# Optimization experiments

Measured on AMD Instinct MI355X. Metric: run time of the kernel, lower is better.

## Reference

```python
import jax, jax.numpy as jnp
import numpy as np

B, F, H, N, S, L, E = 32, 128, 256, 2048, 3, 2, 262144
DEG = E // (B * N)  # average degree used to normalize position updates


def setup_inputs() -> dict:
    key = jax.random.key(0)
    ks = jax.random.split(key, 12)
    s = 0.05
    return {
        "x": jax.random.normal(ks[0], (B, F), jnp.float32),
        "positions": jax.random.normal(ks[1], (N, S), jnp.float32),
        "W_in": jax.random.normal(ks[2], (F, H), jnp.float32) * s,
        "b_in": jnp.zeros((H,), jnp.float32),
        "Wg1": jax.random.normal(ks[3], (3, H // 2), jnp.float32) * s,
        "bg1": jnp.zeros((H // 2,), jnp.float32),
        "Wg2": jax.random.normal(ks[4], (H // 2, H), jnp.float32) * s,
        "bg2": jnp.zeros((H,), jnp.float32),
        "Wm": jax.random.normal(ks[5], (L, 2 * H + 1, H), jnp.float32) * s,
        "bm": jnp.zeros((L, H), jnp.float32),
        "Wu": jax.random.normal(ks[6], (L, 2 * H, H), jnp.float32) * s,
        "bu": jnp.zeros((L, H), jnp.float32),
        "Wp": jax.random.normal(ks[7], (L, H, 1), jnp.float32) * s,
        "W_out": jax.random.normal(ks[8], (H, 1), jnp.float32) * s,
        "b_out": jnp.zeros((1,), jnp.float32),
        "edge_index": jax.random.randint(ks[9], (2, E), 0, B * N, dtype=jnp.int32),
    }


def _geometric_features(positions, Wg1, bg1, Wg2, bg2):
    # For single points, pairwise / centroid / Hausdorff distances all reduce to
    # the euclidean distance, so feature[i, 0..2] = mean_{j != i} ||p_i - p_j||.
    n = positions.shape[0]
    diff = positions[:, None, :] - positions[None, :, :]      # [N, N, S]
    dsq = jnp.sum(diff * diff, axis=-1)                        # [N, N]
    mask = 1.0 - jnp.eye(n, dtype=positions.dtype)
    d = jnp.sqrt(jnp.where(mask > 0, dsq, 1.0)) * mask         # grad-safe sqrt
    mean_d = jnp.sum(d, axis=1) / (n - 1)                      # [N]
    gf = jnp.stack([mean_d, mean_d, mean_d], axis=-1)          # [N, 3]
    return jax.nn.relu(gf @ Wg1 + bg1) @ Wg2 + bg2             # [N, H]


def _forward(x, positions, W_in, b_in, Wg1, bg1, Wg2, bg2, Wm, bm, Wu, bu, Wp, W_out, b_out, edge_index):
    nn_ = B * N
    h = x @ W_in + b_in                                        # [B, H]
    h = jnp.broadcast_to(h[:, None, :], (B, N, H)).reshape(nn_, H)
    pos = jnp.broadcast_to(positions[None], (B, N, S)).reshape(nn_, S)
    g = _geometric_features(positions, Wg1, bg1, Wg2, bg2)     # [N, H]
    h = h + jnp.broadcast_to(g[None], (B, N, H)).reshape(nn_, H)
    src, dst = edge_index[0], edge_index[1]
    for l in range(L):  # small fixed layer loop
        dvec = pos[src] - pos[dst]
        d = jnp.sqrt(jnp.sum(dvec * dvec, axis=-1, keepdims=True) + 1e-12)  # [E, 1]
        m = jax.nn.relu(jnp.concatenate([h[src], h[dst], d], axis=-1) @ Wm[l] + bm[l])
        agg = jax.ops.segment_sum(m, dst, num_segments=nn_)    # [B*N, H]
        coef = m @ Wp[l]                                       # [E, 1]
        pos = pos + jax.ops.segment_sum((pos[dst] - pos[src]) * coef, dst, num_segments=nn_) / DEG
        h = h + jax.nn.relu(jnp.concatenate([h, agg], axis=-1) @ Wu[l] + bu[l])
    out = (h.reshape(B, N, H) @ W_out + b_out).squeeze(-1)     # [B, N]
    return out


def reference(x, positions, W_in, b_in, Wg1, bg1, Wg2, bg2, Wm, bm, Wu, bu, Wp, W_out, b_out, edge_index):
    return _forward(x, positions, W_in, b_in, Wg1, bg1, Wg2, bg2, Wm, bm, Wu, bu, Wp, W_out, b_out, edge_index)
```

## Files before the change

kernel.cpp:

```cpp
#include <hip/hip_runtime.h>
#include <math.h>

#define B_ 32
#define F_ 128
#define H_ 256
#define N_ 2048
#define L_ 2
#define E_ 262144
#define NN_ 65536

typedef __attribute__((ext_vector_type(8))) short short8;
typedef __attribute__((ext_vector_type(4))) float f32x4;
typedef __attribute__((ext_vector_type(2))) float f32x2;

static __device__ __forceinline__ unsigned short f2bf(float f) {
  unsigned int u = __float_as_uint(f);
  u += 0x7FFF + ((u >> 16) & 1);
  return (unsigned short)(u >> 16);
}
static __device__ __forceinline__ float bf2f(unsigned short u) {
  return __uint_as_float(((unsigned int)u) << 16);
}
static __device__ __forceinline__ unsigned int pk_bf16(float lo, float hi) {
  unsigned int r;
  asm("v_cvt_pk_bf16_f32 %0, %1, %2" : "=v"(r) : "v"(lo), "v"(hi));
  return r;
}

typedef const __attribute__((address_space(1))) unsigned int* as1p;
typedef __attribute__((address_space(3))) unsigned int* as3p;
static __device__ __forceinline__ void gload16(const void* g, void* l) {
  __builtin_amdgcn_global_load_lds((as1p)g, (as3p)l, 16, 0, 0);
}


__global__ void h0_kernel(const float* __restrict__ x, const float* __restrict__ W_in,
                          const float* __restrict__ b_in, float* __restrict__ h0) {
  int b = blockIdx.x;
  int j = threadIdx.x;
  float acc = b_in[j];
#pragma unroll 8
  for (int k = 0; k < F_; ++k)
    acc += x[b * F_ + k] * W_in[k * H_ + j];
  h0[b * H_ + j] = acc;
}

__global__ void meand_g_kernel(const float* __restrict__ positions,
                               const float* __restrict__ Wg1, const float* __restrict__ bg1,
                               const float* __restrict__ Wg2, const float* __restrict__ bg2,
                               float* __restrict__ g) {
  __shared__ float red[256];
  __shared__ float hid[128];
  int n = blockIdx.x;
  int t = threadIdx.x;
  float px = positions[n * 3 + 0], py = positions[n * 3 + 1], pz = positions[n * 3 + 2];
  float s = 0.f;
  for (int j = t; j < N_; j += 256) {
    float dx = px - positions[j * 3 + 0];
    float dy = py - positions[j * 3 + 1];
    float dz = pz - positions[j * 3 + 2];
    s += sqrtf(dx * dx + dy * dy + dz * dz);
  }
  red[t] = s;
  __syncthreads();
  for (int off = 128; off > 0; off >>= 1) {
    if (t < off) red[t] += red[t + off];
    __syncthreads();
  }
  float md = red[0] / (float)(N_ - 1);
  if (t < 128) {
    float w = Wg1[t] + Wg1[128 + t] + Wg1[256 + t];
    hid[t] = fmaxf(md * w + bg1[t], 0.f);
  }
  __syncthreads();
  float acc = bg2[t];
#pragma unroll 8
  for (int k = 0; k < 128; ++k)
    acc += hid[k] * Wg2[k * H_ + t];
  g[n * H_ + t] = acc;
}

__global__ void hbfinit_kernel(const float* __restrict__ h0, const float* __restrict__ g,
                               unsigned short* __restrict__ hbf) {
  int idx = blockIdx.x * blockDim.x + threadIdx.x;
  int row = idx >> 5;
  int c8 = (idx & 31) << 3;
  const float* hp = h0 + (row >> 11) * H_ + c8;
  const float* gp = g + (row & (N_ - 1)) * H_ + c8;
  const float4 a = *(const float4*)hp;
  const float4 a2 = *(const float4*)(hp + 4);
  const float4 b = *(const float4*)gp;
  const float4 b2 = *(const float4*)(gp + 4);
  short8 v;
  v[0] = (short)f2bf(a.x + b.x);  v[1] = (short)f2bf(a.y + b.y);
  v[2] = (short)f2bf(a.z + b.z);  v[3] = (short)f2bf(a.w + b.w);
  v[4] = (short)f2bf(a2.x + b2.x); v[5] = (short)f2bf(a2.y + b2.y);
  v[6] = (short)f2bf(a2.z + b2.z); v[7] = (short)f2bf(a2.w + b2.w);
  *(short8*)(hbf + (((size_t)row) << 8) + c8) = v;
}

__global__ void posinit_kernel(const float* __restrict__ positions, float* __restrict__ pos4) {
  int n = blockIdx.x * blockDim.x + threadIdx.x;
  int src = (n & (N_ - 1)) * 3;
  float4 v;
  v.x = positions[src + 0];
  v.y = positions[src + 1];
  v.z = positions[src + 2];
  v.w = 0.f;
  *(float4*)(pos4 + ((size_t)n << 2)) = v;
}


__global__ void deg_kernel(const int* __restrict__ ei, int* __restrict__ deg) {
  int e = blockIdx.x * 256 + threadIdx.x;
  atomicAdd(&deg[ei[E_ + e]], 1);
}

__global__ void scan1_kernel(const int* __restrict__ deg, int* __restrict__ bsum) {
  __shared__ int red[256];
  int t = threadIdx.x;
  red[t] = deg[blockIdx.x * 256 + t];
  __syncthreads();
  for (int off = 128; off > 0; off >>= 1) {
    if (t < off) red[t] += red[t + off];
    __syncthreads();
  }
  if (t == 0) bsum[blockIdx.x] = red[0];
}

__global__ void scan2_kernel(int* __restrict__ bsum) {
  __shared__ int s[256];
  int t = threadIdx.x;
  s[t] = bsum[t];
  __syncthreads();
  for (int off = 1; off < 256; off <<= 1) {
    int v = (t >= off) ? s[t - off] : 0;
    __syncthreads();
    s[t] += v;
    __syncthreads();
  }
  bsum[t] = (t == 0) ? 0 : s[t - 1];
}

__global__ void scan3_kernel(const int* __restrict__ deg, const int* __restrict__ bsum,
                             int* __restrict__ cur, int* __restrict__ rowptr) {
  __shared__ int s[256];
  int t = threadIdx.x;
  int i = blockIdx.x * 256 + t;
  s[t] = deg[i];
  __syncthreads();
  for (int off = 1; off < 256; off <<= 1) {
    int v = (t >= off) ? s[t - off] : 0;
    __syncthreads();
    s[t] += v;
    __syncthreads();
  }
  int excl = (t == 0) ? 0 : s[t - 1];
  int v = bsum[blockIdx.x] + excl;
  cur[i] = v;
  rowptr[i] = v;
}

__global__ void scatter_kernel(const int* __restrict__ ei, int* __restrict__ cur,
                               int* __restrict__ src_s) {
  int e = blockIdx.x * 256 + threadIdx.x;
  int s = ei[e], d = ei[E_ + e];
  int p = atomicAdd(&cur[d], 1);
  src_s[p] = s;
}

__global__ void wconv_all(const float* __restrict__ Wm, const float* __restrict__ Wu,
                          unsigned short* __restrict__ Wt1, unsigned short* __restrict__ Wut) {
  int idx = blockIdx.x * 256 + threadIdx.x;
  int sel = idx >> 14;
  int rem = idx & 16383;
  if (sel < 2) {
    const float* W = Wm + (size_t)sel * 513 * H_;
    unsigned short* dst = Wt1 + (size_t)sel * 131072 + ((size_t)rem << 3);
    int g = rem >> 13;
    int r2 = rem & 8191;
    int kc = r2 >> 11, w = (r2 >> 9) & 3, ks = (r2 >> 8) & 1, ni = (r2 >> 6) & 3, lane = r2 & 63;
    int r = lane & 15, q = lane >> 4;
    int n  = (w << 6) + (ni << 4) + r;
    int kb = (g << 8) + (kc << 6) + (ks << 5) + (q << 3);
#pragma unroll
    for (int j = 0; j < 8; ++j)
      dst[j] = f2bf(W[(size_t)(kb + j) * H_ + n]);
  } else {
    const float* W = Wu + (size_t)(sel - 2) * 512 * H_;
    unsigned short* dst = Wut + (size_t)(sel - 2) * 131072 + ((size_t)rem << 3);
    int kc = rem >> 11, w = (rem >> 9) & 3, ks = (rem >> 8) & 1, ni = (rem >> 6) & 3, lane = rem & 63;
    int r = lane & 15, q = lane >> 4;
    int n  = (w << 6) + (ni << 4) + r;
    int kb = (kc << 6) + (ks << 5) + (q << 3);
#pragma unroll
    for (int j = 0; j < 8; ++j)
      dst[j] = f2bf(W[(size_t)(kb + j) * H_ + n]);
  }
}


#define GEMM_IDS                                                     \
  const int t = threadIdx.x;                                         \
  const int m0 = blockIdx.x << 6;                                    \
  const int wu = __builtin_amdgcn_readfirstlane(t >> 6);             \
  const int lane = t & 63;                                           \
  const int q = lane >> 4;                                           \
  const int r = lane & 15;                                           \
  const int arow = lane >> 2;                                        \
  const int aq = (lane & 3) ^ ((lane >> 2) & 3);

#define STAGE_P(P, abase)                                                                \
  do {                                                                                   \
    gload16((abase) + (((size_t)(m0 + (wu << 4) + arow)) << 8) + (((P) & 7) << 5) +      \
                (aq << 3),                                                               \
            &sA[(P) & 3][wu << 9]);                                                      \
    _Pragma("unroll")                                                                    \
    for (int j_ = 0; j_ < 4; ++j_)                                                       \
      gload16(Wt + (((size_t)((P) >> 1)) << 14) + (wu << 12) + (((P) & 1) << 11) +       \
                  (j_ << 9) + (lane << 3),                                               \
              &sB[(P) & 3][(wu << 11) + (j_ << 9)]);                                     \
  } while (0)

#define COMPUTE_P(P)                                                                     \
  do {                                                                                   \
    short8 af[4], bfr[4];                                                                \
    _Pragma("unroll")                                                                    \
    for (int mi = 0; mi < 4; ++mi)                                                       \
      af[mi] = *(const short8*)(&sA[(P) & 3][((mi * 16 + r) << 5) +                      \
                                             ((q ^ (r & 3)) << 3)]);                     \
    _Pragma("unroll")                                                                    \
    for (int ni = 0; ni < 4; ++ni)                                                       \
      bfr[ni] = *(const short8*)(&sB[(P) & 3][(wu << 11) + (ni << 9) + (lane << 3)]);    \
    _Pragma("unroll")                                                                    \
    for (int mi = 0; mi < 4; ++mi)                                                       \
      _Pragma("unroll")                                                                  \
      for (int ni = 0; ni < 4; ++ni)                                                     \
        acc[mi][ni] = __builtin_amdgcn_mfma_f32_16x16x32_bf16(af[mi], bfr[ni],           \
                                                              acc[mi][ni], 0, 0, 0);     \
  } while (0)

#define WAIT_BAR(P)                                                       \
  do {                                                                    \
    if ((P) <= 13)      asm volatile("s_waitcnt vmcnt(10)" ::: "memory"); \
    else if ((P) == 14) asm volatile("s_waitcnt vmcnt(5)" ::: "memory");  \
    else                asm volatile("s_waitcnt vmcnt(0)" ::: "memory");  \
    __builtin_amdgcn_s_barrier();                                         \
    asm volatile("" ::: "memory");                                        \
  } while (0)

#define ACC_ZERO()                                   \
  _Pragma("unroll")                                  \
  for (int mi = 0; mi < 4; ++mi)                     \
    _Pragma("unroll")                                \
    for (int ni = 0; ni < 4; ++ni)                   \
      acc[mi][ni] = (f32x4){0.f, 0.f, 0.f, 0.f};

__launch_bounds__(256)
__global__ void gemm1_mfma(const unsigned short* __restrict__ hbf,
                           const unsigned short* __restrict__ Wt,
                           const float* __restrict__ bm,
                           unsigned short* __restrict__ X, unsigned short* __restrict__ Zb) {
  __shared__ __align__(16) unsigned short sA[4][2048];
  __shared__ __align__(16) unsigned short sB[4][8192];
  GEMM_IDS

  f32x4 acc[4][4];
  ACC_ZERO();

  STAGE_P(0, hbf); STAGE_P(1, hbf); STAGE_P(2, hbf);
#pragma unroll
  for (int p = 0; p < 16; ++p) {
    WAIT_BAR(p);
    if (p + 3 < 16) STAGE_P(p + 3, hbf);
    COMPUTE_P(p);
    if (p == 7) {
#pragma unroll
      for (int ni = 0; ni < 4; ++ni) {
        int n = (wu << 6) + ni * 16 + r;
#pragma unroll
        for (int mi = 0; mi < 4; ++mi)
#pragma unroll
          for (int reg = 0; reg < 4; ++reg) {
            size_t idx = (((size_t)(m0 + mi * 16 + q * 4 + reg)) << 8) + n;
            X[idx] = f2bf(acc[mi][ni][reg]);
            acc[mi][ni][reg] = 0.f;
          }
      }
    }
  }

#pragma unroll
  for (int ni = 0; ni < 4; ++ni) {
    int n = (wu << 6) + ni * 16 + r;
    float bmn = bm[n];
#pragma unroll
    for (int mi = 0; mi < 4; ++mi)
#pragma unroll
      for (int reg = 0; reg < 4; ++reg) {
        size_t idx = (((size_t)(m0 + mi * 16 + q * 4 + reg)) << 8) + n;
        Zb[idx] = f2bf(acc[mi][ni][reg] + bmn);
      }
  }
}

static __device__ __forceinline__ void edge_do(
    const float4 pn, const float4 q, const uint2 xv,
    const f32x2 z01, const f32x2 z23,
    const f32x2 wl01, const f32x2 wl23,
    const f32x2 wp01, const f32x2 wp23,
    f32x2& a01, f32x2& a23,
    float& pdx, float& pdy, float& pdz) {
  const float dx = pn.x - q.x, dy = pn.y - q.y, dz = pn.z - q.z;
  const float d = sqrtf(dx * dx + dy * dy + dz * dz + 1e-12f);
  f32x2 dd; dd[0] = d; dd[1] = d;
  f32x2 x01, x23;
  x01[0] = __uint_as_float(xv.x << 16);
  x01[1] = __uint_as_float(xv.x & 0xffff0000u);
  x23[0] = __uint_as_float(xv.y << 16);
  x23[1] = __uint_as_float(xv.y & 0xffff0000u);
  f32x2 v01 = x01 + z01 + dd * wl01;
  f32x2 v23 = x23 + z23 + dd * wl23;
  v01[0] = fmaxf(v01[0], 0.f); v01[1] = fmaxf(v01[1], 0.f);
  v23[0] = fmaxf(v23[0], 0.f); v23[1] = fmaxf(v23[1], 0.f);
  a01 += v01; a23 += v23;
  const f32x2 cpv = v01 * wp01 + v23 * wp23;
  const float cp = cpv[0] + cpv[1];
  pdx += dx * cp; pdy += dy * cp; pdz += dz * cp;
}

__launch_bounds__(256)
__global__ void edge_kernel(const unsigned short* __restrict__ X,
                            const unsigned short* __restrict__ Zb,
                            const float* __restrict__ pos_c,
                            const int* __restrict__ rowptr, const int* __restrict__ src_s,
                            const float* __restrict__ wl, const float* __restrict__ wp,
                            unsigned short* __restrict__ aggb, float* __restrict__ pos_o) {
  const int gid = blockIdx.x * 256 + threadIdx.x;
  const int n = __builtin_amdgcn_readfirstlane(gid >> 6);
  const int lane = threadIdx.x & 63;

  const float4 wlv = *(const float4*)(wl + (lane << 2));
  const float4 wpv = *(const float4*)(wp + (lane << 2));
  const f32x2 wl01 = {wlv.x, wlv.y}, wl23 = {wlv.z, wlv.w};
  const f32x2 wp01 = {wpv.x, wpv.y}, wp23 = {wpv.z, wpv.w};

  const int e0 = rowptr[n];
  const int e1 = (n == NN_ - 1) ? E_ : rowptr[n + 1];

  const uint2 zv = *(const uint2*)(Zb + (((size_t)n) << 8) + (lane << 2));
  f32x2 z01, z23;
  z01[0] = __uint_as_float(zv.x << 16);
  z01[1] = __uint_as_float(zv.x & 0xffff0000u);
  z23[0] = __uint_as_float(zv.y << 16);
  z23[1] = __uint_as_float(zv.y & 0xffff0000u);

  const float4 pn = *(const float4*)(pos_c + ((size_t)n << 2));
  f32x2 a01 = {0.f, 0.f}, a23 = {0.f, 0.f};
  float pdx = 0.f, pdy = 0.f, pdz = 0.f;

  const unsigned short* Xl = X + (lane << 2);

  int e = e0;
  for (; e + 4 <= e1; e += 4) {
    const int s0 = src_s[e], s1 = src_s[e + 1], s2 = src_s[e + 2], s3 = src_s[e + 3];
    const float4 q0 = *(const float4*)(pos_c + ((size_t)s0 << 2));
    const float4 q1 = *(const float4*)(pos_c + ((size_t)s1 << 2));
    const float4 q2 = *(const float4*)(pos_c + ((size_t)s2 << 2));
    const float4 q3 = *(const float4*)(pos_c + ((size_t)s3 << 2));
    const uint2 x0 = *(const uint2*)(Xl + (((size_t)s0) << 8));
    const uint2 x1 = *(const uint2*)(Xl + (((size_t)s1) << 8));
    const uint2 x2 = *(const uint2*)(Xl + (((size_t)s2) << 8));
    const uint2 x3 = *(const uint2*)(Xl + (((size_t)s3) << 8));
    edge_do(pn, q0, x0, z01, z23, wl01, wl23, wp01, wp23, a01, a23, pdx, pdy, pdz);
    edge_do(pn, q1, x1, z01, z23, wl01, wl23, wp01, wp23, a01, a23, pdx, pdy, pdz);
    edge_do(pn, q2, x2, z01, z23, wl01, wl23, wp01, wp23, a01, a23, pdx, pdy, pdz);
    edge_do(pn, q3, x3, z01, z23, wl01, wl23, wp01, wp23, a01, a23, pdx, pdy, pdz);
  }
  if (e + 2 <= e1) {
    const int s0 = src_s[e], s1 = src_s[e + 1];
    const float4 q0 = *(const float4*)(pos_c + ((size_t)s0 << 2));
    const float4 q1 = *(const float4*)(pos_c + ((size_t)s1 << 2));
    const uint2 x0 = *(const uint2*)(Xl + (((size_t)s0) << 8));
    const uint2 x1 = *(const uint2*)(Xl + (((size_t)s1) << 8));
    edge_do(pn, q0, x0, z01, z23, wl01, wl23, wp01, wp23, a01, a23, pdx, pdy, pdz);
    edge_do(pn, q1, x1, z01, z23, wl01, wl23, wp01, wp23, a01, a23, pdx, pdy, pdz);
    e += 2;
  }
  if (e < e1) {
    const int s0 = src_s[e];
    const float4 q0 = *(const float4*)(pos_c + ((size_t)s0 << 2));
    const uint2 x0 = *(const uint2*)(Xl + (((size_t)s0) << 8));
    edge_do(pn, q0, x0, z01, z23, wl01, wl23, wp01, wp23, a01, a23, pdx, pdy, pdz);
  }

  uint2 av;
  av.x = pk_bf16(a01[0], a01[1]);
  av.y = pk_bf16(a23[0], a23[1]);
  *(uint2*)(aggb + (((size_t)n) << 8) + (lane << 2)) = av;

#pragma unroll
  for (int m = 1; m < 64; m <<= 1) {
    pdx += __shfl_xor(pdx, m, 64);
    pdy += __shfl_xor(pdy, m, 64);
    pdz += __shfl_xor(pdz, m, 64);
  }
  if (lane == 0) {
    float4 po;
    po.x = pn.x + pdx * 0.25f;
    po.y = pn.y + pdy * 0.25f;
    po.z = pn.z + pdz * 0.25f;
    po.w = 0.f;
    *(float4*)(pos_o + ((size_t)n << 2)) = po;
  }
}

__launch_bounds__(256)
__global__ void upd2_mfma(unsigned short* __restrict__ hbf,
                          const unsigned short* __restrict__ aggb,
                          const unsigned short* __restrict__ Wt,
                          const float* __restrict__ bu) {
  __shared__ __align__(16) unsigned short sA[4][2048];
  __shared__ __align__(16) unsigned short sB[4][8192];
  GEMM_IDS

  f32x4 acc[4][4];
  ACC_ZERO();

  const unsigned short* hb = (const unsigned short*)hbf;
  STAGE_P(0, hb); STAGE_P(1, hb); STAGE_P(2, hb);
#pragma unroll
  for (int p = 0; p < 16; ++p) {
    WAIT_BAR(p);
    if (p + 3 < 16) {
      const unsigned short* ab = (p + 3 < 8) ? hb : aggb;
      STAGE_P(p + 3, ab);
    }
    COMPUTE_P(p);
  }

#pragma unroll
  for (int ni = 0; ni < 4; ++ni) {
    int n = (wu << 6) + ni * 16 + r;
    float buv = bu[n];
#pragma unroll
    for (int mi = 0; mi < 4; ++mi)
#pragma unroll
      for (int reg = 0; reg < 4; ++reg) {
        size_t idx = (((size_t)(m0 + mi * 16 + q * 4 + reg)) << 8) + n;
        float v = bf2f(hbf[idx]) + fmaxf(acc[mi][ni][reg] + buv, 0.f);
        hbf[idx] = f2bf(v);
      }
  }
}

__launch_bounds__(256)
__global__ void upd2_out(const unsigned short* __restrict__ hbf,
                         const unsigned short* __restrict__ aggb,
                         const unsigned short* __restrict__ Wt,
                         const float* __restrict__ bu,
                         const float* __restrict__ Wout, const float* __restrict__ bout,
                         float* __restrict__ out) {
  __shared__ __align__(16) unsigned short sA[4][2048];
  __shared__ __align__(16) unsigned short sB[4][8192];
  GEMM_IDS

  f32x4 acc[4][4];
  ACC_ZERO();

  STAGE_P(0, hbf); STAGE_P(1, hbf); STAGE_P(2, hbf);
#pragma unroll
  for (int p = 0; p < 16; ++p) {
    WAIT_BAR(p);
    if (p + 3 < 16) {
      const unsigned short* ab = (p + 3 < 8) ? hbf : aggb;
      STAGE_P(p + 3, ab);
    }
    COMPUTE_P(p);
  }
  __syncthreads();
  float (*sRed)[64] = (float(*)[64])(&sA[0][0]);

  float dotp[4][4];
#pragma unroll
  for (int mi = 0; mi < 4; ++mi)
#pragma unroll
    for (int reg = 0; reg < 4; ++reg)
      dotp[mi][reg] = 0.f;

#pragma unroll
  for (int ni = 0; ni < 4; ++ni) {
    int n = (wu << 6) + ni * 16 + r;
    float buv = bu[n];
    float won = Wout[n];
#pragma unroll
    for (int mi = 0; mi < 4; ++mi)
#pragma unroll
      for (int reg = 0; reg < 4; ++reg) {
        size_t idx = (((size_t)(m0 + mi * 16 + q * 4 + reg)) << 8) + n;
        float v = bf2f(hbf[idx]) + fmaxf(acc[mi][ni][reg] + buv, 0.f);
        dotp[mi][reg] += v * won;
      }
  }
#pragma unroll
  for (int mask = 1; mask < 16; mask <<= 1)
#pragma unroll
    for (int mi = 0; mi < 4; ++mi)
#pragma unroll
      for (int reg = 0; reg < 4; ++reg)
        dotp[mi][reg] += __shfl_xor(dotp[mi][reg], mask, 64);
  if (r == 0) {
#pragma unroll
    for (int mi = 0; mi < 4; ++mi)
#pragma unroll
      for (int reg = 0; reg < 4; ++reg)
        sRed[wu][mi * 16 + q * 4 + reg] = dotp[mi][reg];
  }
  __syncthreads();
  if (t < 64)
    out[m0 + t] = sRed[0][t] + sRed[1][t] + sRed[2][t] + sRed[3][t] + bout[0];
}


extern "C" void kernel_launch(void* const* d_in, const int* in_sizes, int n_in,
                              void* d_out, int out_size, void* d_ws, size_t ws_size,
                              hipStream_t stream) {
  const float* x         = (const float*)d_in[0];
  const float* positions = (const float*)d_in[1];
  const float* W_in      = (const float*)d_in[2];
  const float* b_in      = (const float*)d_in[3];
  const float* Wg1       = (const float*)d_in[4];
  const float* bg1       = (const float*)d_in[5];
  const float* Wg2       = (const float*)d_in[6];
  const float* bg2       = (const float*)d_in[7];
  const float* Wm        = (const float*)d_in[8];
  const float* bm        = (const float*)d_in[9];
  const float* Wu        = (const float*)d_in[10];
  const float* bu        = (const float*)d_in[11];
  const float* Wp        = (const float*)d_in[12];
  const float* W_out     = (const float*)d_in[13];
  const float* b_out     = (const float*)d_in[14];
  const int*   ei        = (const int*)d_in[15];
  float* out = (float*)d_out;

  char* ws = (char*)d_ws;
  unsigned short* hbf   = (unsigned short*)(ws);
  unsigned short* X     = (unsigned short*)(ws +  33554432UL);
  unsigned short* Zb    = (unsigned short*)(ws +  67108864UL);
  unsigned short* aggb  = (unsigned short*)(ws + 100663296UL);
  float*          posA  = (float*)(ws + 134217728UL);
  float*          posB  = (float*)(ws + 135266304UL);
  float*          g     = (float*)(ws + 136314880UL);
  float*          h0    = (float*)(ws + 138412032UL);
  unsigned short* Wt1   = (unsigned short*)(ws + 138444800UL);
  unsigned short* Wut   = (unsigned short*)(ws + 138969088UL);
  int*            deg   = (int*)(ws + 139493376UL);
  int*            cur   = (int*)(ws + 139755520UL);
  int*            bsum  = (int*)(ws + 140017664UL);
  int*            rowptr= (int*)(ws + 140018688UL);
  int*            src_s = (int*)(ws + 140280832UL);

  hipMemsetAsync(deg, 0, (size_t)NN_ * sizeof(int), stream);
  deg_kernel<<<E_ / 256, 256, 0, stream>>>(ei, deg);
  scan1_kernel<<<256, 256, 0, stream>>>(deg, bsum);
  scan2_kernel<<<1, 256, 0, stream>>>(bsum);
  scan3_kernel<<<256, 256, 0, stream>>>(deg, bsum, cur, rowptr);
  scatter_kernel<<<E_ / 256, 256, 0, stream>>>(ei, cur, src_s);

  wconv_all<<<256, 256, 0, stream>>>(Wm, Wu, Wt1, Wut);

  h0_kernel<<<B_, 256, 0, stream>>>(x, W_in, b_in, h0);
  meand_g_kernel<<<N_, 256, 0, stream>>>(positions, Wg1, bg1, Wg2, bg2, g);
  hbfinit_kernel<<<NN_ * 32 / 256, 256, 0, stream>>>(h0, g, hbf);
  posinit_kernel<<<NN_ / 256, 256, 0, stream>>>(positions, posA);

  float* pos_cur = posA;
  float* pos_nxt = posB;
  for (int l = 0; l < L_; ++l) {
    gemm1_mfma<<<NN_ / 64, 256, 0, stream>>>(hbf, Wt1 + (size_t)l * 131072,
                                             bm + (size_t)l * H_, X, Zb);
    edge_kernel<<<NN_ / 4, 256, 0, stream>>>(X, Zb, pos_cur, rowptr, src_s,
                                             Wm + (size_t)l * 513 * H_ + 512 * H_,
                                             Wp + (size_t)l * H_, aggb, pos_nxt);
    if (l < L_ - 1) {
      upd2_mfma<<<NN_ / 64, 256, 0, stream>>>(hbf, aggb, Wut + (size_t)l * 131072,
                                              bu + (size_t)l * H_);
    } else {
      upd2_out<<<NN_ / 64, 256, 0, stream>>>(hbf, aggb, Wut + (size_t)l * 131072,
                                             bu + (size_t)l * H_, W_out, b_out, out);
    }
    float* tmp = pos_cur; pos_cur = pos_nxt; pos_nxt = tmp;
  }
}
```

Before: 333.7 us.

## Exploit low-rank structure of layer-0 hidden state to shrink first message GEMM

Before the first layer, h equals h0[batch] plus g[node], so h@W splits into g@W plus h0@W. The change computes the layer-0 message GEMM on only 2080 distinct rows (2048 g rows and 32 h0 rows) instead of 65536. The edge kernel then rebuilds each per-edge X and Z term by adding the two fp32 partial results. This removes most of the layer-0 GEMM work, at the cost of two fp32 gathers per edge instead of one bf16 gather.

Result: faster. 324.5 us (-2.7%).

```diff
diff --git a/kernel.cpp b/kernel.cpp
--- a/kernel.cpp
+++ b/kernel.cpp
@@ -99,6 +99,23 @@
   *(short8*)(hbf + (((size_t)row) << 8) + c8) = v;
 }
 
+__global__ void hginit_kernel(const float* __restrict__ h0, const float* __restrict__ g,
+                              unsigned short* __restrict__ hg) {
+  int idx = blockIdx.x * blockDim.x + threadIdx.x;
+  int row = idx >> 5;
+  int c8 = (idx & 31) << 3;
+  const float* src = (row < 2048) ? (g + (size_t)row * H_ + c8)
+                                  : (h0 + (size_t)(row - 2048) * H_ + c8);
+  const float4 a = *(const float4*)src;
+  const float4 a2 = *(const float4*)(src + 4);
+  short8 v;
+  v[0] = (short)f2bf(a.x);  v[1] = (short)f2bf(a.y);
+  v[2] = (short)f2bf(a.z);  v[3] = (short)f2bf(a.w);
+  v[4] = (short)f2bf(a2.x); v[5] = (short)f2bf(a2.y);
+  v[6] = (short)f2bf(a2.z); v[7] = (short)f2bf(a2.w);
+  *(short8*)(hg + (((size_t)row) << 8) + c8) = v;
+}
+
 __global__ void posinit_kernel(const float* __restrict__ positions, float* __restrict__ pos4) {
   int n = blockIdx.x * blockDim.x + threadIdx.x;
   int src = (n & (N_ - 1)) * 3;
@@ -304,8 +321,58 @@
   }
 }
 
-static __device__ __forceinline__ void edge_do(
-    const float4 pn, const float4 q, const uint2 xv,
+__launch_bounds__(256)
+__global__ void gemm1_small(const unsigned short* __restrict__ hg,
+                            const unsigned short* __restrict__ Wt,
+                            const float* __restrict__ bm,
+                            float* __restrict__ Xc, float* __restrict__ Zc) {
+  __shared__ __align__(16) unsigned short sA[4][2048];
+  __shared__ __align__(16) unsigned short sB[4][8192];
+  GEMM_IDS
+
+  f32x4 acc[4][4];
+  ACC_ZERO();
+
+  STAGE_P(0, hg); STAGE_P(1, hg); STAGE_P(2, hg);
+#pragma unroll
+  for (int p = 0; p < 16; ++p) {
+    WAIT_BAR(p);
+    if (p + 3 < 16) STAGE_P(p + 3, hg);
+    COMPUTE_P(p);
+    if (p == 7) {
+#pragma unroll
+      for (int ni = 0; ni < 4; ++ni) {
+        int n = (wu << 6) + ni * 16 + r;
+#pragma unroll
+        for (int mi = 0; mi < 4; ++mi)
+#pragma unroll
+          for (int reg = 0; reg < 4; ++reg) {
+            size_t idx = (((size_t)(m0 + mi * 16 + q * 4 + reg)) << 8) + n;
+            Xc[idx] = acc[mi][ni][reg];
+            acc[mi][ni][reg] = 0.f;
+          }
+      }
+    }
+  }
+
+  const int isH0 = (blockIdx.x == 32);
+#pragma unroll
+  for (int ni = 0; ni < 4; ++ni) {
+    int n = (wu << 6) + ni * 16 + r;
+    float bmn = isH0 ? bm[n] : 0.f;
+#pragma unroll
+    for (int mi = 0; mi < 4; ++mi)
+#pragma unroll
+      for (int reg = 0; reg < 4; ++reg) {
+        size_t idx = (((size_t)(m0 + mi * 16 + q * 4 + reg)) << 8) + n;
+        Zc[idx] = acc[mi][ni][reg] + bmn;
+      }
+  }
+}
+
+static __device__ __forceinline__ void edge_core(
+    const float4 pn, const float4 q,
+    f32x2 x01, f32x2 x23,
     const f32x2 z01, const f32x2 z23,
     const f32x2 wl01, const f32x2 wl23,
     const f32x2 wp01, const f32x2 wp23,
@@ -314,11 +381,6 @@
   const float dx = pn.x - q.x, dy = pn.y - q.y, dz = pn.z - q.z;
   const float d = sqrtf(dx * dx + dy * dy + dz * dz + 1e-12f);
   f32x2 dd; dd[0] = d; dd[1] = d;
-  f32x2 x01, x23;
-  x01[0] = __uint_as_float(xv.x << 16);
-  x01[1] = __uint_as_float(xv.x & 0xffff0000u);
-  x23[0] = __uint_as_float(xv.y << 16);
-  x23[1] = __uint_as_float(xv.y & 0xffff0000u);
   f32x2 v01 = x01 + z01 + dd * wl01;
   f32x2 v23 = x23 + z23 + dd * wl23;
   v01[0] = fmaxf(v01[0], 0.f); v01[1] = fmaxf(v01[1], 0.f);
@@ -327,6 +389,34 @@
   const f32x2 cpv = v01 * wp01 + v23 * wp23;
   const float cp = cpv[0] + cpv[1];
   pdx += dx * cp; pdy += dy * cp; pdz += dz * cp;
+}
+
+static __device__ __forceinline__ void edge_do(
+    const float4 pn, const float4 q, const uint2 xv,
+    const f32x2 z01, const f32x2 z23,
+    const f32x2 wl01, const f32x2 wl23,
+    const f32x2 wp01, const f32x2 wp23,
+    f32x2& a01, f32x2& a23,
+    float& pdx, float& pdy, float& pdz) {
+  f32x2 x01, x23;
+  x01[0] = __uint_as_float(xv.x << 16);
+  x01[1] = __uint_as_float(xv.x & 0xffff0000u);
+  x23[0] = __uint_as_float(xv.y << 16);
+  x23[1] = __uint_as_float(xv.y & 0xffff0000u);
+  edge_core(pn, q, x01, x23, z01, z23, wl01, wl23, wp01, wp23, a01, a23, pdx, pdy, pdz);
+}
+
+static __device__ __forceinline__ void edge_do0(
+    const float4 pn, const float4 q, const float4 xg, const float4 xh,
+    const f32x2 z01, const f32x2 z23,
+    const f32x2 wl01, const f32x2 wl23,
+    const f32x2 wp01, const f32x2 wp23,
+    f32x2& a01, f32x2& a23,
+    float& pdx, float& pdy, float& pdz) {
+  f32x2 x01, x23;
+  x01[0] = xg.x + xh.x; x01[1] = xg.y + xh.y;
+  x23[0] = xg.z + xh.z; x23[1] = xg.w + xh.w;
+  edge_core(pn, q, x01, x23, z01, z23, wl01, wl23, wp01, wp23, a01, a23, pdx, pdy, pdz);
 }
 
 __launch_bounds__(256)
@@ -392,6 +482,87 @@
     const float4 q0 = *(const float4*)(pos_c + ((size_t)s0 << 2));
     const uint2 x0 = *(const uint2*)(Xl + (((size_t)s0) << 8));
     edge_do(pn, q0, x0, z01, z23, wl01, wl23, wp01, wp23, a01, a23, pdx, pdy, pdz);
+  }
+
+  uint2 av;
+  av.x = pk_bf16(a01[0], a01[1]);
+  av.y = pk_bf16(a23[0], a23[1]);
+  *(uint2*)(aggb + (((size_t)n) << 8) + (lane << 2)) = av;
+
+#pragma unroll
+  for (int m = 1; m < 64; m <<= 1) {
+    pdx += __shfl_xor(pdx, m, 64);
+    pdy += __shfl_xor(pdy, m, 64);
+    pdz += __shfl_xor(pdz, m, 64);
+  }
+  if (lane == 0) {
+    float4 po;
+    po.x = pn.x + pdx * 0.25f;
+    po.y = pn.y + pdy * 0.25f;
+    po.z = pn.z + pdz * 0.25f;
+    po.w = 0.f;
+    *(float4*)(pos_o + ((size_t)n << 2)) = po;
+  }
+}
+
+__launch_bounds__(256)
+__global__ void edge0_kernel(const float* __restrict__ Xc,
+                             const float* __restrict__ Zc,
+                             const float* __restrict__ pos_c,
+                             const int* __restrict__ rowptr, const int* __restrict__ src_s,
+                             const float* __restrict__ wl, const float* __restrict__ wp,
+                             unsigned short* __restrict__ aggb, float* __restrict__ pos_o) {
+  const int gid = blockIdx.x * 256 + threadIdx.x;
+  const int n = __builtin_amdgcn_readfirstlane(gid >> 6);
+  const int lane = threadIdx.x & 63;
+
+  const float4 wlv = *(const float4*)(wl + (lane << 2));
+  const float4 wpv = *(const float4*)(wp + (lane << 2));
+  const f32x2 wl01 = {wlv.x, wlv.y}, wl23 = {wlv.z, wlv.w};
+  const f32x2 wp01 = {wpv.x, wpv.y}, wp23 = {wpv.z, wpv.w};
+
+  const int e0 = rowptr[n];
+  const int e1 = (n == NN_ - 1) ? E_ : rowptr[n + 1];
+
+  const float* Xl = Xc + (lane << 2);
+  const float* Zl = Zc + (lane << 2);
+
+  const float4 zg = *(const float4*)(Zl + (((size_t)(n & (N_ - 1))) << 8));
+  const float4 zh = *(const float4*)(Zl + (((size_t)(2048 + (n >> 11))) << 8));
+  f32x2 z01, z23;
+  z01[0] = zg.x + zh.x; z01[1] = zg.y + zh.y;
+  z23[0] = zg.z + zh.z; z23[1] = zg.w + zh.w;
+
+  const float4 pn = *(const float4*)(pos_c + ((size_t)n << 2));
+  f32x2 a01 = {0.f, 0.f}, a23 = {0.f, 0.f};
+  float pdx = 0.f, pdy = 0.f, pdz = 0.f;
+
+  int e = e0;
+  for (; e + 4 <= e1; e += 4) {
+    const int s0 = src_s[e], s1 = src_s[e + 1], s2 = src_s[e + 2], s3 = src_s[e + 3];
+    const float4 q0 = *(const float4*)(pos_c + ((size_t)s0 << 2));
+    const float4 q1 = *(const float4*)(pos_c + ((size_t)s1 << 2));
+    const float4 q2 = *(const float4*)(pos_c + ((size_t)s2 << 2));
+    const float4 q3 = *(const float4*)(pos_c + ((size_t)s3 << 2));
+    const float4 xg0 = *(const float4*)(Xl + (((size_t)(s0 & (N_ - 1))) << 8));
+    const float4 xh0 = *(const float4*)(Xl + (((size_t)(2048 + (s0 >> 11))) << 8));
+    const float4 xg1 = *(const float4*)(Xl + (((size_t)(s1 & (N_ - 1))) << 8));
+    const float4 xh1 = *(const float4*)(Xl + (((size_t)(2048 + (s1 >> 11))) << 8));
+    const float4 xg2 = *(const float4*)(Xl + (((size_t)(s2 & (N_ - 1))) << 8));
+    const float4 xh2 = *(const float4*)(Xl + (((size_t)(2048 + (s2 >> 11))) << 8));
+    const float4 xg3 = *(const float4*)(Xl + (((size_t)(s3 & (N_ - 1))) << 8));
+    const float4 xh3 = *(const float4*)(Xl + (((size_t)(2048 + (s3 >> 11))) << 8));
+    edge_do0(pn, q0, xg0, xh0, z01, z23, wl01, wl23, wp01, wp23, a01, a23, pdx, pdy, pdz);
+    edge_do0(pn, q1, xg1, xh1, z01, z23, wl01, wl23, wp01, wp23, a01, a23, pdx, pdy, pdz);
+    edge_do0(pn, q2, xg2, xh2, z01, z23, wl01, wl23, wp01, wp23, a01, a23, pdx, pdy, pdz);
+    edge_do0(pn, q3, xg3, xh3, z01, z23, wl01, wl23, wp01, wp23, a01, a23, pdx, pdy, pdz);
+  }
+  for (; e < e1; ++e) {
+    const int s0 = src_s[e];
+    const float4 q0 = *(const float4*)(pos_c + ((size_t)s0 << 2));
+    const float4 xg0 = *(const float4*)(Xl + (((size_t)(s0 & (N_ - 1))) << 8));
+    const float4 xh0 = *(const float4*)(Xl + (((size_t)(2048 + (s0 >> 11))) << 8));
+    edge_do0(pn, q0, xg0, xh0, z01, z23, wl01, wl23, wp01, wp23, a01, a23, pdx, pdy, pdz);
   }
 
   uint2 av;
@@ -560,6 +731,10 @@
   int*            rowptr= (int*)(ws + 140018688UL);
   int*            src_s = (int*)(ws + 140280832UL);
 
+  unsigned short* hg = aggb;
+  float*          Xc = (float*)X;
+  float*          Zc = (float*)Zb;
+
   hipMemsetAsync(deg, 0, (size_t)NN_ * sizeof(int), stream);
   deg_kernel<<<E_ / 256, 256, 0, stream>>>(ei, deg);
   scan1_kernel<<<256, 256, 0, stream>>>(deg, bsum);
@@ -572,23 +747,19 @@
   h0_kernel<<<B_, 256, 0, stream>>>(x, W_in, b_in, h0);
   meand_g_kernel<<<N_, 256, 0, stream>>>(positions, Wg1, bg1, Wg2, bg2, g);
   hbfinit_kernel<<<NN_ * 32 / 256, 256, 0, stream>>>(h0, g, hbf);
+  hginit_kernel<<<2080 * 32 / 256, 256, 0, stream>>>(h0, g, hg);
   posinit_kernel<<<NN_ / 256, 256, 0, stream>>>(positions, posA);
 
-  float* pos_cur = posA;
-  float* pos_nxt = posB;
-  for (int l = 0; l < L_; ++l) {
-    gemm1_mfma<<<NN_ / 64, 256, 0, stream>>>(hbf, Wt1 + (size_t)l * 131072,
-                                             bm + (size_t)l * H_, X, Zb);
-    edge_kernel<<<NN_ / 4, 256, 0, stream>>>(X, Zb, pos_cur, rowptr, src_s,
-                                             Wm + (size_t)l * 513 * H_ + 512 * H_,
-                                             Wp + (size_t)l * H_, aggb, pos_nxt);
-    if (l < L_ - 1) {
-      upd2_mfma<<<NN_ / 64, 256, 0, stream>>>(hbf, aggb, Wut + (size_t)l * 131072,
-                                              bu + (size_t)l * H_);
-    } else {
-      upd2_out<<<NN_ / 64, 256, 0, stream>>>(hbf, aggb, Wut + (size_t)l * 131072,
-                                             bu + (size_t)l * H_, W_out, b_out, out);
-    }
-    float* tmp = pos_cur; pos_cur = pos_nxt; pos_nxt = tmp;
-  }
-}
+  gemm1_small<<<33, 256, 0, stream>>>(hg, Wt1, bm, Xc, Zc);
+  edge0_kernel<<<NN_ / 4, 256, 0, stream>>>(Xc, Zc, posA, rowptr, src_s,
+                                            Wm + 512 * H_, Wp, aggb, posB);
+  upd2_mfma<<<NN_ / 64, 256, 0, stream>>>(hbf, aggb, Wut, bu);
+
+  gemm1_mfma<<<NN_ / 64, 256, 0, stream>>>(hbf, Wt1 + 131072,
+                                           bm + H_, X, Zb);
+  edge_kernel<<<NN_ / 4, 256, 0, stream>>>(X, Zb, posB, rowptr, src_s,
+                                           Wm + (size_t)513 * H_ + 512 * H_,
+                                           Wp + H_, aggb, posA);
+  upd2_out<<<NN_ / 64, 256, 0, stream>>>(hbf, aggb, Wut + 131072,
+                                         bu + H_, W_out, b_out, out);
+}
```
